# Kernel tuning notes

Measured on AMD Instinct MI355X. Metric: run time of the kernel, lower is better.

## Reference

```python
import jax, jax.numpy as jnp
import numpy as np

WS = 7          # window_size (square)
HEADS = 12


def _relative_position_index(ws=WS):
    # Faithful port of WindowAttentionBase._get_relative_position_index
    coords = np.stack(np.meshgrid(np.arange(ws), np.arange(ws), indexing='ij'))  # [2, ws, ws]
    flat = coords.reshape(2, -1)                       # [2, n]
    rel = flat[:, :, None] - flat[:, None, :]          # [2, n, n]
    rel = rel.transpose(1, 2, 0)                       # [n, n, 2]
    rel[:, :, 0] += ws - 1
    rel[:, :, 1] += ws - 1
    rel[:, :, 0] *= 2 * ws - 1
    return jnp.asarray(rel.sum(-1).reshape(-1), dtype=jnp.int32)  # [n*n]


def setup_inputs() -> dict:
    key = jax.random.key(0)
    ks = jax.random.split(key, 6)
    b, H, W, c = 32, 56, 56, 384
    return {
        "x": jax.random.normal(ks[0], (b, H, W, c), jnp.float32),
        "w_qkv": jax.random.normal(ks[1], (3 * c, c), jnp.float32) * (c ** -0.5),
        "b_qkv": jax.random.normal(ks[2], (3 * c,), jnp.float32) * 0.02,
        "rel_pos": jax.random.normal(ks[3], (HEADS, (2 * WS - 1) ** 2), jnp.float32),
        "w_out": jax.random.normal(ks[4], (c, c), jnp.float32) * (c ** -0.5),
        "b_out": jax.random.normal(ks[5], (c,), jnp.float32) * 0.02,
    }


def reference(x, w_qkv, b_qkv, rel_pos, w_out, b_out):
    b, H, W, c = x.shape
    g = HEADS
    d = c // g
    hn, wn = H // WS, W // WS
    n = WS * WS
    scale = d ** -0.5

    # split_into_windows: 'b (p h) (q w) c -> b h w (p q) c'  (p,q = window dims, OUTER factors)
    xw = x.reshape(b, WS, hn, WS, wn, c).transpose(0, 2, 4, 1, 3, 5).reshape(b, hn, wn, n, c)

    qkv = xw @ w_qkv.T + b_qkv                          # [b, hn, wn, n, 3c]
    q, k, v = jnp.split(qkv, 3, axis=-1)
    # 'b h w n (g d) -> b g h w n d'
    to_heads = lambda t: t.reshape(b, hn, wn, n, g, d).transpose(0, 4, 1, 2, 3, 5)
    q, k, v = to_heads(q) * scale, to_heads(k), to_heads(v)

    sim = jnp.einsum('bghwnd,bghwmd->bghwnm', q, k)     # [b, g, hn, wn, n, n]
    idx = _relative_position_index()
    bias = rel_pos[:, idx].reshape(g, n, n)             # gather relative position bias
    sim = sim + bias[None, :, None, None, :, :]

    attn = jax.nn.softmax(sim, axis=-1)
    out = jnp.einsum('bghwnm,bghwmd->bghwnd', attn, v)  # [b, g, hn, wn, n, d]

    # 'b g h w n d -> b h w n (g d)' then merge_windows 'b h w (p q) c -> b (p h) (q w) c'
    out = out.transpose(0, 2, 3, 4, 1, 5).reshape(b, hn, wn, n, c)
    out = out.reshape(b, hn, wn, WS, WS, c).transpose(0, 3, 1, 4, 2, 5).reshape(b, H, W, c)
    return out @ w_out.T + b_out
```

## Files before the change

### kernel.cpp

```cpp
#include <hip/hip_runtime.h>

typedef __attribute__((ext_vector_type(8))) short bf16x8;
typedef __attribute__((ext_vector_type(4))) float f32x4;

__device__ __forceinline__ unsigned short f2bf(float f){
  unsigned u = __builtin_bit_cast(unsigned, f);
  u += 0x7fffu + ((u >> 16) & 1u);
  return (unsigned short)(u >> 16);
}

__device__ __forceinline__ unsigned cvt_pk_bf16(float lo, float hi){
  unsigned r;
  asm("v_cvt_pk_bf16_f32 %0, %1, %2" : "=v"(r) : "v"(lo), "v"(hi));
  return r;
}

#define ASYNC16(ldsp, gp) __builtin_amdgcn_global_load_lds( \
    (const __attribute__((address_space(1))) unsigned int*)(gp), \
    (__attribute__((address_space(3))) unsigned int*)(ldsp), 16, 0, 0)

__global__ __launch_bounds__(256) void convert_x_kernel(const float* __restrict__ x,
                                                        unsigned short* __restrict__ xb){
  int idx = blockIdx.x*256 + threadIdx.x;
  int token = idx / 96, j = idx - token*96;
  int b = token / 3136, rem = token - b*3136;
  int rr = rem / 56, cp = rem - rr*56;
  int p = rr >> 3, h = rr & 7, q = cp >> 3, w = cp & 7;
  int orow = ((b*8 + h)*8 + w)*49 + p*7 + q;
  float4 v = *(const float4*)(x + (size_t)idx*4);
  ushort4 o;
  o.x = f2bf(v.x); o.y = f2bf(v.y); o.z = f2bf(v.z); o.w = f2bf(v.w);
  *(ushort4*)(xb + (size_t)orow*384 + j*4) = o;
}

__global__ __launch_bounds__(256) void convert_w_kernel(const float* __restrict__ wq,
                                                        const float* __restrict__ wo,
                                                        unsigned short* __restrict__ wqb,
                                                        unsigned short* __restrict__ wob){
  int idx = blockIdx.x*256 + threadIdx.x;
  if (idx < 110592){
    float4 v = *(const float4*)(wq + (size_t)idx*4);
    ushort4 o; o.x=f2bf(v.x); o.y=f2bf(v.y); o.z=f2bf(v.z); o.w=f2bf(v.w);
    *(ushort4*)(wqb + (size_t)idx*4) = o;
  } else {
    int k = idx - 110592;
    float4 v = *(const float4*)(wo + (size_t)k*4);
    ushort4 o; o.x=f2bf(v.x); o.y=f2bf(v.y); o.z=f2bf(v.z); o.w=f2bf(v.w);
    *(ushort4*)(wob + (size_t)k*4) = o;
  }
}

__global__ __launch_bounds__(256) void build_btab(const float* __restrict__ rel_pos,
                                                  float* __restrict__ btab){
  int idx = blockIdx.x*256 + threadIdx.x;
  int head = idx >> 10, rem = idx & 1023;
  int fi = rem >> 6, lane = rem & 63;
  int ti = fi >> 2, tj = fi & 3;
  int qq = tj*16 + (lane & 15);
  int kb = ti*16 + (lane >> 4)*4;
  float4 v; float* vp = (float*)&v;
#pragma unroll
  for (int r=0; r<4; ++r){
    int kk = kb + r;
    float val;
    if (kk >= 49) val = -__builtin_inff();
    else if (qq >= 49) val = 0.f;
    else {
      int ip = qq/7, iq = qq - ip*7, jp = kk/7, jq = kk - jp*7;
      val = rel_pos[head*169 + (ip-jp+6)*13 + (iq-jq+6)] * 1.4426950408889634f;
    }
    vp[r] = val;
  }
  *(float4*)(btab + (size_t)idx*4) = v;
}

template<int EPI, int NBY>
__global__ __launch_bounds__(256) void gemm256(const unsigned short* __restrict__ A,
                                               const unsigned short* __restrict__ B,
                                               const float* __restrict__ bias,
                                               unsigned short* __restrict__ qo,
                                               unsigned short* __restrict__ ko,
                                               unsigned short* __restrict__ vo,
                                               float* __restrict__ out)
{
  constexpr int K = 384;
  constexpr int NT = 12;
  __shared__ unsigned short Al[3][256*32];
  __shared__ unsigned short Bl[3][128*32];
  const int tid = threadIdx.x;
  const int lane = tid & 63, wid = tid >> 6;
  const int wr = wid >> 1, wc = wid & 1;
  const int l15 = lane & 15, kg = lane >> 4;
  const int swz = (l15 >> 1) & 3;
  const int cswz = (tid & 3) ^ ((tid >> 3) & 3);

  const int n = blockIdx.x;
  const int xcd = n & 7, s = n >> 3;
  const int panel = s / NBY, nb = s - panel*NBY;
  const int bx = panel*8 + xcd, by = nb;

  const unsigned short* Ag = A + ((size_t)bx*256 + (tid>>2))*K + cswz*8;
  const unsigned short* Bg = B + ((size_t)(by*128 + (tid>>2)))*K + cswz*8;

  f32x4 acc[8][4] = {};

#define STAGE(buf, kt) do { \
    ASYNC16(&Al[buf][wid*512],        Ag + (kt)*32); \
    ASYNC16(&Al[buf][wid*512 + 2048], Ag + (size_t)64*K  + (kt)*32); \
    ASYNC16(&Al[buf][wid*512 + 4096], Ag + (size_t)128*K + (kt)*32); \
    ASYNC16(&Al[buf][wid*512 + 6144], Ag + (size_t)192*K + (kt)*32); \
    ASYNC16(&Bl[buf][wid*512],        Bg + (kt)*32); \
    ASYNC16(&Bl[buf][wid*512 + 2048], Bg + (size_t)64*K  + (kt)*32); \
  } while(0)

  STAGE(0,0); STAGE(1,1);

#pragma unroll
  for (int t = 0; t < NT; ++t){
    if (t < NT-1) asm volatile("s_waitcnt vmcnt(6)\n\ts_barrier" ::: "memory");
    else          asm volatile("s_waitcnt vmcnt(0)\n\ts_barrier" ::: "memory");

    if (t + 2 < NT) STAGE((t+2)%3, t+2);

    const unsigned short* Ab = Al[t % 3];
    const unsigned short* Bb = Bl[t % 3];
    bf16x8 af[8], bfv[4];
#pragma unroll
    for (int ti=0; ti<8; ++ti)
      af[ti] = *(const bf16x8*)(Ab + (wr*128 + ti*16 + l15)*32 + (kg ^ swz)*8);
#pragma unroll
    for (int tj=0; tj<4; ++tj)
      bfv[tj] = *(const bf16x8*)(Bb + (wc*64 + tj*16 + l15)*32 + (kg ^ swz)*8);

    __builtin_amdgcn_s_setprio(1);
#pragma unroll
    for (int ti=0; ti<8; ++ti)
#pragma unroll
      for (int tj=0; tj<4; ++tj)
        acc[ti][tj] = __builtin_amdgcn_mfma_f32_16x16x32_bf16(af[ti], bfv[tj], acc[ti][tj], 0,0,0);
    __builtin_amdgcn_s_setprio(0);
  }
#undef STAGE

  const int rbase = bx*256 + wr*128 + kg*4;

  if (EPI == 0){
    const int t = by / 3;
    unsigned short* __restrict__ Pout = (t==0) ? qo : ((t==1) ? ko : vo);
    const float scale = (t==0) ? (0.17677669529663689f * 1.4426950408889634f) : 1.0f;
    const int cb = (by - t*3)*128 + wc*64;
    int hoff[4]; float bvs[4];
#pragma unroll
    for (int tj=0; tj<4; ++tj){
      int colt = cb + tj*16;
      hoff[tj] = (colt>>5)*1568 + (colt&31) + l15;
      bvs[tj] = bias[by*128 + wc*64 + tj*16 + l15] * scale;
    }
#pragma unroll
    for (int ti=0; ti<8; ++ti){
#pragma unroll
      for (int r=0; r<4; ++r){
        int R = rbase + ti*16 + r;
        int win = R / 49, nn = R - win*49;
        size_t rowoff = (size_t)win*18816 + nn*32;
#pragma unroll
        for (int tj=0; tj<4; ++tj)
          Pout[rowoff + hoff[tj]] = f2bf(acc[ti][tj][r]*scale + bvs[tj]);
      }
    }
  } else {
    const int cbs = by*128 + wc*64;
    float bv[4];
#pragma unroll
    for (int tj=0; tj<4; ++tj) bv[tj] = bias[cbs + tj*16 + l15];
#pragma unroll
    for (int ti=0; ti<8; ++ti){
#pragma unroll
      for (int r=0; r<4; ++r){
        int R = rbase + ti*16 + r;
        int win = R / 49, nn = R - win*49;
        int p = nn / 7, q = nn - p*7;
        int h = (win >> 3) & 7, w = win & 7;
        size_t tok = (size_t)(win >> 6)*3136 + (size_t)((p*8 + h)*56 + q*8 + w);
        float* __restrict__ orow = out + tok*384 + cbs + l15;
#pragma unroll
        for (int tj=0; tj<4; ++tj)
          orow[tj*16] = acc[ti][tj][r] + bv[tj];
      }
    }
  }
}

__global__ __launch_bounds__(256) void attn_kernel(const unsigned short* __restrict__ q,
                                                   const unsigned short* __restrict__ k,
                                                   const unsigned short* __restrict__ v,
                                                   const float* __restrict__ btab,
                                                   unsigned short* __restrict__ ao)
{
  __shared__ unsigned short P[4][4096];
  const int tid = threadIdx.x, lane = tid & 63, wid = tid >> 6;
  const int l15 = lane & 15, kg = lane >> 4;
  const int win = blockIdx.x / 3;
  const int head = (blockIdx.x % 3)*4 + wid;
  const size_t base = ((size_t)win*12 + head)*1568;
  const unsigned short* qb = q + base;
  const unsigned short* kb = k + base;
  const unsigned short* vb = v + base;
  const float* bt = btab + head*4096;

  bf16x8 vfk[2][2];
#pragma unroll
  for (int ks=0; ks<2; ++ks)
#pragma unroll
    for (int tjv=0; tjv<2; ++tjv)
#pragma unroll
      for (int e=0; e<8; ++e)
        vfk[ks][tjv][e] = (short)vb[(ks*32 + kg*8 + e)*32 + tjv*16 + l15];

  f32x4 s[4][4];
#pragma unroll
  for (int ti=0; ti<4; ++ti)
#pragma unroll
    for (int tj=0; tj<4; ++tj)
      s[ti][tj] = *(const f32x4*)(bt + ((ti*4 + tj)*64 + lane)*4);

  bf16x8 kf[4], qf[4];
#pragma unroll
  for (int ti=0; ti<4; ++ti) kf[ti] = *(const bf16x8*)(kb + (ti*16+l15)*32 + kg*8);
#pragma unroll
  for (int tj=0; tj<4; ++tj) qf[tj] = *(const bf16x8*)(qb + (tj*16+l15)*32 + kg*8);

  __builtin_amdgcn_s_setprio(1);
#pragma unroll
  for (int ti=0; ti<4; ++ti)
#pragma unroll
    for (int tj=0; tj<4; ++tj)
      s[ti][tj] = __builtin_amdgcn_mfma_f32_16x16x32_bf16(kf[ti], qf[tj], s[ti][tj], 0,0,0);
  __builtin_amdgcn_s_setprio(0);

  float rinv[4];
#pragma unroll
  for (int tj=0; tj<4; ++tj){
    float sum = 0.f;
#pragma unroll
    for (int ti=0; ti<4; ++ti)
#pragma unroll
      for (int r=0; r<4; ++r){
        float e = exp2f(s[ti][tj][r]);
        s[ti][tj][r] = e;
        sum += e;
      }
    sum += __shfl_xor(sum, 16);
    sum += __shfl_xor(sum, 32);
    rinv[tj] = __builtin_amdgcn_rcpf(sum);
  }

  unsigned short* Pl = P[wid];
  const unsigned swz = (unsigned)((l15 & 7) << 4);
#pragma unroll
  for (int tj=0; tj<4; ++tj){
    const float rv = rinv[tj];
    const unsigned rowb = (unsigned)((tj*16 + l15)*128);
#pragma unroll
    for (int ti=0; ti<4; ++ti){
      uint2 d;
      d.x = cvt_pk_bf16(s[ti][tj][0]*rv, s[ti][tj][1]*rv);
      d.y = cvt_pk_bf16(s[ti][tj][2]*rv, s[ti][tj][3]*rv);
      unsigned boff = (rowb + (unsigned)(ti*32 + kg*8)) ^ swz;
      *(uint2*)((char*)Pl + boff) = d;
    }
  }

  f32x4 o[4][2] = {};
#pragma unroll
  for (int oti=0; oti<4; ++oti){
    bf16x8 pa[2];
#pragma unroll
    for (int ks=0; ks<2; ++ks){
      unsigned boff = ((unsigned)((oti*16+l15)*128 + ks*64 + kg*16)) ^ swz;
      pa[ks] = *(const bf16x8*)((char*)Pl + boff);
    }
    __builtin_amdgcn_s_setprio(1);
#pragma unroll
    for (int tjv=0; tjv<2; ++tjv){
      o[oti][tjv] = __builtin_amdgcn_mfma_f32_16x16x32_bf16(pa[0], vfk[0][tjv], o[oti][tjv], 0,0,0);
      o[oti][tjv] = __builtin_amdgcn_mfma_f32_16x16x32_bf16(pa[1], vfk[1][tjv], o[oti][tjv], 0,0,0);
    }
    __builtin_amdgcn_s_setprio(0);
  }

#pragma unroll
  for (int oti=0; oti<4; ++oti)
#pragma unroll
    for (int r=0; r<4; ++r){
      int row = oti*16 + kg*4 + r;
      if (row < 49){
        unsigned short* op = ao + ((size_t)win*49 + row)*384 + head*32 + l15;
        op[0]  = (unsigned short)cvt_pk_bf16(o[oti][0][r], o[oti][0][r]);
        op[16] = (unsigned short)cvt_pk_bf16(o[oti][1][r], o[oti][1][r]);
      }
    }
}

extern "C" void kernel_launch(void* const* d_in, const int* in_sizes, int n_in,
                              void* d_out, int out_size, void* d_ws, size_t ws_size,
                              hipStream_t stream)
{
  const float* x       = (const float*)d_in[0];
  const float* w_qkv   = (const float*)d_in[1];
  const float* b_qkv   = (const float*)d_in[2];
  const float* rel_pos = (const float*)d_in[3];
  const float* w_out   = (const float*)d_in[4];
  const float* b_out   = (const float*)d_in[5];
  float* out = (float*)d_out;

  char* ws = (char*)d_ws;
  unsigned short* wqb = (unsigned short*)ws;
  unsigned short* wob = (unsigned short*)(ws + 884736);
  float* btab         = (float*)(ws + 884736 + 294912);
  unsigned short* qws = (unsigned short*)(ws + 1376256);
  unsigned short* kws = qws + 38535168;
  unsigned short* vws = kws + 38535168;
  unsigned short* xb  = vws + 38535168;
  unsigned short* ao  = xb;

  convert_x_kernel<<<dim3(37632), dim3(256), 0, stream>>>(x, xb);
  convert_w_kernel<<<dim3(576),   dim3(256), 0, stream>>>(w_qkv, w_out, wqb, wob);
  build_btab<<<dim3(48), dim3(256), 0, stream>>>(rel_pos, btab);
  gemm256<0,9><<<dim3(3528), dim3(256), 0, stream>>>(xb, wqb, b_qkv, qws, kws, vws, nullptr);
  attn_kernel<<<dim3(6144), dim3(256), 0, stream>>>(qws, kws, vws, btab, ao);
  gemm256<1,3><<<dim3(1176), dim3(256), 0, stream>>>(ao, wob, b_out, nullptr, nullptr, nullptr, out);
}
```

Baseline: 308.1 us.

## Process two windows per attention block with prefetch of second window's Q/K/V

Each attention workgroup now handles two consecutive windows instead of one, halving the grid size. The second window's Q, K and V fragments are loaded from global memory before the first window's softmax and PV stage, so their latency can hide behind that compute. This costs more registers per thread, which may lower occupancy, and leaves fewer blocks to spread across the device.

```diff
diff --git a/kernel.cpp b/kernel.cpp
--- a/kernel.cpp
+++ b/kernel.cpp
@@ -191,6 +191,81 @@
   }
 }
 
+#define ATTN_QK(KF, QF) do { \
+  _Pragma("unroll") \
+  for (int ti=0; ti<4; ++ti) \
+    _Pragma("unroll") \
+    for (int tj=0; tj<4; ++tj) \
+      s[ti][tj] = *(const f32x4*)(bt + ((ti*4 + tj)*64 + lane)*4); \
+  __builtin_amdgcn_s_setprio(1); \
+  _Pragma("unroll") \
+  for (int ti=0; ti<4; ++ti) \
+    _Pragma("unroll") \
+    for (int tj=0; tj<4; ++tj) \
+      s[ti][tj] = __builtin_amdgcn_mfma_f32_16x16x32_bf16(KF[ti], QF[tj], s[ti][tj], 0,0,0); \
+  __builtin_amdgcn_s_setprio(0); \
+} while(0)
+
+#define ATTN_TAIL(VV, WADD) do { \
+  float rinv[4]; \
+  _Pragma("unroll") \
+  for (int tj=0; tj<4; ++tj){ \
+    float sum = 0.f; \
+    _Pragma("unroll") \
+    for (int ti=0; ti<4; ++ti) \
+      _Pragma("unroll") \
+      for (int r=0; r<4; ++r){ \
+        float e = exp2f(s[ti][tj][r]); \
+        s[ti][tj][r] = e; \
+        sum += e; \
+      } \
+    sum += __shfl_xor(sum, 16); \
+    sum += __shfl_xor(sum, 32); \
+    rinv[tj] = __builtin_amdgcn_rcpf(sum); \
+  } \
+  _Pragma("unroll") \
+  for (int tj=0; tj<4; ++tj){ \
+    const float rv = rinv[tj]; \
+    const unsigned rowb = (unsigned)((tj*16 + l15)*128); \
+    _Pragma("unroll") \
+    for (int ti=0; ti<4; ++ti){ \
+      uint2 d; \
+      d.x = cvt_pk_bf16(s[ti][tj][0]*rv, s[ti][tj][1]*rv); \
+      d.y = cvt_pk_bf16(s[ti][tj][2]*rv, s[ti][tj][3]*rv); \
+      unsigned boff = (rowb + (unsigned)(ti*32 + kg*8)) ^ swzP; \
+      *(uint2*)((char*)Pl + boff) = d; \
+    } \
+  } \
+  f32x4 o[4][2] = {}; \
+  _Pragma("unroll") \
+  for (int oti=0; oti<4; ++oti){ \
+    bf16x8 pa[2]; \
+    _Pragma("unroll") \
+    for (int ks=0; ks<2; ++ks){ \
+      unsigned boff = ((unsigned)((oti*16+l15)*128 + ks*64 + kg*16)) ^ swzP; \
+      pa[ks] = *(const bf16x8*)((char*)Pl + boff); \
+    } \
+    __builtin_amdgcn_s_setprio(1); \
+    _Pragma("unroll") \
+    for (int tjv=0; tjv<2; ++tjv){ \
+      o[oti][tjv] = __builtin_amdgcn_mfma_f32_16x16x32_bf16(pa[0], VV[0][tjv], o[oti][tjv], 0,0,0); \
+      o[oti][tjv] = __builtin_amdgcn_mfma_f32_16x16x32_bf16(pa[1], VV[1][tjv], o[oti][tjv], 0,0,0); \
+    } \
+    __builtin_amdgcn_s_setprio(0); \
+  } \
+  _Pragma("unroll") \
+  for (int oti=0; oti<4; ++oti) \
+    _Pragma("unroll") \
+    for (int r=0; r<4; ++r){ \
+      int row = oti*16 + kg*4 + r; \
+      if (row < 49){ \
+        unsigned short* op = ao + ((size_t)(win0 + (WADD))*49 + row)*384 + head*32 + l15; \
+        op[0]  = (unsigned short)cvt_pk_bf16(o[oti][0][r], o[oti][0][r]); \
+        op[16] = (unsigned short)cvt_pk_bf16(o[oti][1][r], o[oti][1][r]); \
+      } \
+    } \
+} while(0)
+
 __global__ __launch_bounds__(256) void attn_kernel(const unsigned short* __restrict__ q,
                                                    const unsigned short* __restrict__ k,
                                                    const unsigned short* __restrict__ v,
@@ -200,106 +275,52 @@
   __shared__ unsigned short P[4][4096];
   const int tid = threadIdx.x, lane = tid & 63, wid = tid >> 6;
   const int l15 = lane & 15, kg = lane >> 4;
-  const int win = blockIdx.x / 3;
   const int head = (blockIdx.x % 3)*4 + wid;
-  const size_t base = ((size_t)win*12 + head)*1568;
-  const unsigned short* qb = q + base;
-  const unsigned short* kb = k + base;
-  const unsigned short* vb = v + base;
+  const int win0 = (blockIdx.x / 3)*2;
+  const size_t base0 = ((size_t)win0*12 + head)*1568;
+  const unsigned short* qb = q + base0;
+  const unsigned short* kb = k + base0;
+  const unsigned short* vb = v + base0;
   const float* bt = btab + head*4096;
-
-  bf16x8 vfk[2][2];
+  unsigned short* Pl = P[wid];
+  const unsigned swzP = (unsigned)((l15 & 7) << 4);
+  constexpr int WOFF = 12*1568;
+
+  f32x4 s[4][4];
+  bf16x8 vA[2][2], vB[2][2], kfA[4], qfA[4], kfB[4], qfB[4];
+
 #pragma unroll
   for (int ks=0; ks<2; ++ks)
 #pragma unroll
     for (int tjv=0; tjv<2; ++tjv)
 #pragma unroll
       for (int e=0; e<8; ++e)
-        vfk[ks][tjv][e] = (short)vb[(ks*32 + kg*8 + e)*32 + tjv*16 + l15];
-
-  f32x4 s[4][4];
-#pragma unroll
-  for (int ti=0; ti<4; ++ti)
-#pragma unroll
-    for (int tj=0; tj<4; ++tj)
-      s[ti][tj] = *(const f32x4*)(bt + ((ti*4 + tj)*64 + lane)*4);
-
-  bf16x8 kf[4], qf[4];
-#pragma unroll
-  for (int ti=0; ti<4; ++ti) kf[ti] = *(const bf16x8*)(kb + (ti*16+l15)*32 + kg*8);
-#pragma unroll
-  for (int tj=0; tj<4; ++tj) qf[tj] = *(const bf16x8*)(qb + (tj*16+l15)*32 + kg*8);
-
-  __builtin_amdgcn_s_setprio(1);
-#pragma unroll
-  for (int ti=0; ti<4; ++ti)
-#pragma unroll
-    for (int tj=0; tj<4; ++tj)
-      s[ti][tj] = __builtin_amdgcn_mfma_f32_16x16x32_bf16(kf[ti], qf[tj], s[ti][tj], 0,0,0);
-  __builtin_amdgcn_s_setprio(0);
-
-  float rinv[4];
-#pragma unroll
-  for (int tj=0; tj<4; ++tj){
-    float sum = 0.f;
-#pragma unroll
-    for (int ti=0; ti<4; ++ti)
-#pragma unroll
-      for (int r=0; r<4; ++r){
-        float e = exp2f(s[ti][tj][r]);
-        s[ti][tj][r] = e;
-        sum += e;
-      }
-    sum += __shfl_xor(sum, 16);
-    sum += __shfl_xor(sum, 32);
-    rinv[tj] = __builtin_amdgcn_rcpf(sum);
-  }
-
-  unsigned short* Pl = P[wid];
-  const unsigned swz = (unsigned)((l15 & 7) << 4);
-#pragma unroll
-  for (int tj=0; tj<4; ++tj){
-    const float rv = rinv[tj];
-    const unsigned rowb = (unsigned)((tj*16 + l15)*128);
-#pragma unroll
-    for (int ti=0; ti<4; ++ti){
-      uint2 d;
-      d.x = cvt_pk_bf16(s[ti][tj][0]*rv, s[ti][tj][1]*rv);
-      d.y = cvt_pk_bf16(s[ti][tj][2]*rv, s[ti][tj][3]*rv);
-      unsigned boff = (rowb + (unsigned)(ti*32 + kg*8)) ^ swz;
-      *(uint2*)((char*)Pl + boff) = d;
-    }
-  }
-
-  f32x4 o[4][2] = {};
-#pragma unroll
-  for (int oti=0; oti<4; ++oti){
-    bf16x8 pa[2];
-#pragma unroll
-    for (int ks=0; ks<2; ++ks){
-      unsigned boff = ((unsigned)((oti*16+l15)*128 + ks*64 + kg*16)) ^ swz;
-      pa[ks] = *(const bf16x8*)((char*)Pl + boff);
-    }
-    __builtin_amdgcn_s_setprio(1);
-#pragma unroll
-    for (int tjv=0; tjv<2; ++tjv){
-      o[oti][tjv] = __builtin_amdgcn_mfma_f32_16x16x32_bf16(pa[0], vfk[0][tjv], o[oti][tjv], 0,0,0);
-      o[oti][tjv] = __builtin_amdgcn_mfma_f32_16x16x32_bf16(pa[1], vfk[1][tjv], o[oti][tjv], 0,0,0);
-    }
-    __builtin_amdgcn_s_setprio(0);
-  }
-
-#pragma unroll
-  for (int oti=0; oti<4; ++oti)
-#pragma unroll
-    for (int r=0; r<4; ++r){
-      int row = oti*16 + kg*4 + r;
-      if (row < 49){
-        unsigned short* op = ao + ((size_t)win*49 + row)*384 + head*32 + l15;
-        op[0]  = (unsigned short)cvt_pk_bf16(o[oti][0][r], o[oti][0][r]);
-        op[16] = (unsigned short)cvt_pk_bf16(o[oti][1][r], o[oti][1][r]);
-      }
-    }
+        vA[ks][tjv][e] = (short)vb[(ks*32 + kg*8 + e)*32 + tjv*16 + l15];
+#pragma unroll
+  for (int i=0; i<4; ++i){
+    kfA[i] = *(const bf16x8*)(kb + (i*16+l15)*32 + kg*8);
+    qfA[i] = *(const bf16x8*)(qb + (i*16+l15)*32 + kg*8);
+  }
+
+  ATTN_QK(kfA, qfA);
+
+#pragma unroll
+  for (int ks=0; ks<2; ++ks)
+#pragma unroll
+    for (int tjv=0; tjv<2; ++tjv)
+#pragma unroll
+      for (int e=0; e<8; ++e)
+        vB[ks][tjv][e] = (short)vb[WOFF + (ks*32 + kg*8 + e)*32 + tjv*16 + l15];
+#pragma unroll
+  for (int i=0; i<4; ++i){
+    kfB[i] = *(const bf16x8*)(kb + WOFF + (i*16+l15)*32 + kg*8);
+    qfB[i] = *(const bf16x8*)(qb + WOFF + (i*16+l15)*32 + kg*8);
+  }
+
+  ATTN_TAIL(vA, 0);
+
+  ATTN_QK(kfB, qfB);
+  ATTN_TAIL(vB, 1);
 }
 
 extern "C" void kernel_launch(void* const* d_in, const int* in_sizes, int n_in,
@@ -328,6 +349,6 @@
   convert_w_kernel<<<dim3(576),   dim3(256), 0, stream>>>(w_qkv, w_out, wqb, wob);
   build_btab<<<dim3(48), dim3(256), 0, stream>>>(rel_pos, btab);
   gemm256<0,9><<<dim3(3528), dim3(256), 0, stream>>>(xb, wqb, b_qkv, qws, kws, vws, nullptr);
-  attn_kernel<<<dim3(6144), dim3(256), 0, stream>>>(qws, kws, vws, btab, ao);
+  attn_kernel<<<dim3(3072), dim3(256), 0, stream>>>(qws, kws, vws, btab, ao);
   gemm256<1,3><<<dim3(1176), dim3(256), 0, stream>>>(ao, wob, b_out, nullptr, nullptr, nullptr, out);
 }
```

Measured after the change: 315.4 us. 2.4% more time.
